# Kernel tuning notes

Measured on AMD Instinct MI355X. Metric: run time of the kernel, lower is better.

Reference implementation:

```python
import math
import jax, jax.numpy as jnp
import numpy as np

D_MODEL = 1024
N_HEADS = 16
D_K = D_MODEL // N_HEADS
THETA = 10000.0
B, S = 2, 2048


def setup_inputs() -> dict:
    key = jax.random.key(0)
    k1, k2, k3 = jax.random.split(key, 3)
    x = jax.random.normal(k1, (B, S, D_MODEL), dtype=jnp.float32)
    token_positions = jnp.arange(B * S, dtype=jnp.int32).reshape(B, S)
    std_qkv = math.sqrt(2.0 / (D_MODEL + 3 * D_MODEL))
    std_o = math.sqrt(2.0 / (D_MODEL + D_MODEL))
    W_qkv = jax.random.truncated_normal(k2, -3.0, 3.0, (3 * D_MODEL, D_MODEL), dtype=jnp.float32) * std_qkv
    W_o = jax.random.truncated_normal(k3, -3.0, 3.0, (D_MODEL, D_MODEL), dtype=jnp.float32) * std_o
    return {"x": x, "W_qkv": W_qkv, "W_o": W_o, "token_positions": token_positions}


def _rope(x, pos):
    # x: (B, H, S, D_K); pos: (B, S) int
    half = D_K // 2
    inv_freq = 1.0 / (THETA ** (jnp.arange(0, D_K, 2, dtype=jnp.float32) / D_K))  # (half,)
    # pos_extended = pos[:, None, :] -> freqs (B, 1, S, half)
    freqs = pos[:, None, :, None].astype(jnp.float32) * inv_freq
    cos, sin = jnp.cos(freqs), jnp.sin(freqs)
    xr = x.reshape(*x.shape[:-1], half, 2)
    x1, x2 = xr[..., 0], xr[..., 1]
    out = jnp.stack([x1 * cos - x2 * sin, x2 * cos + x1 * sin], axis=-1)
    return out.reshape(x.shape)


def reference(x, W_qkv, W_o, token_positions):
    seq_len = x.shape[-2]
    qkv = jnp.einsum('bsi,oi->bso', x, W_qkv)
    q, k, v = jnp.split(qkv, 3, axis=-1)
    # (B, S, H*D) -> (B, H, S, D)
    def to_heads(t):
        return t.reshape(t.shape[0], t.shape[1], N_HEADS, D_K).transpose(0, 2, 1, 3)
    q, k, v = to_heads(q), to_heads(k), to_heads(v)
    q = _rope(q, token_positions)
    k = _rope(k, token_positions)
    scores = jnp.einsum('bhnd,bhmd->bhnm', q, k) / math.sqrt(D_K)
    causal = jnp.tril(jnp.ones((seq_len, seq_len), dtype=bool))
    scores = jnp.where(causal, scores, -jnp.inf)
    attn = jax.nn.softmax(scores, axis=-1)
    out = jnp.einsum('bhnm,bhmd->bhnd', attn, v)
    out = out.transpose(0, 2, 1, 3).reshape(x.shape[0], seq_len, D_MODEL)
    return jnp.einsum('bsi,oi->bso', out, W_o)
```

## Files before the change

kernel.cpp:

```cpp
#include <hip/hip_runtime.h>
#include <cmath>

typedef __bf16 bf16;
typedef bf16 bf16x4 __attribute__((ext_vector_type(4)));
typedef bf16 bf16x8 __attribute__((ext_vector_type(8)));
typedef float f32x4 __attribute__((ext_vector_type(4)));

#define MFMA16(a, b, c) __builtin_amdgcn_mfma_f32_16x16x32_bf16(a, b, c, 0, 0, 0)

#define GLOAD16(g, l)                                                   \
  __builtin_amdgcn_global_load_lds(                                     \
      (const __attribute__((address_space(1))) unsigned int*)(g),       \
      (__attribute__((address_space(3))) unsigned int*)(l), 16, 0, 0)

__global__ __launch_bounds__(256) void cvt_all(
    const float* __restrict__ x, const float* __restrict__ wqkv,
    const float* __restrict__ wo, bf16* __restrict__ xb,
    bf16* __restrict__ wqkvb, bf16* __restrict__ wob) {
  int i = (blockIdx.x * 256 + threadIdx.x) * 4;
  const float* src;
  bf16* dst;
  if (i < (4 << 20)) {
    src = x + i; dst = xb + i;
  } else if (i < (7 << 20)) {
    src = wqkv + (i - (4 << 20)); dst = wqkvb + (i - (4 << 20));
  } else {
    src = wo + (i - (7 << 20)); dst = wob + (i - (7 << 20));
  }
  const f32x4 v = *(const f32x4*)src;
  bf16x4 o = {(bf16)v[0], (bf16)v[1], (bf16)v[2], (bf16)v[3]};
  *(bf16x4*)dst = o;
}

template <int EPI, int BN>
__global__ __launch_bounds__(256) void gemm_nt(
    const bf16* __restrict__ A, const bf16* __restrict__ Bm,
    const int* __restrict__ tokpos,
    bf16* __restrict__ out0, bf16* __restrict__ out1, bf16* __restrict__ out2,
    float* __restrict__ outF, int N) {
  constexpr int NI = BN / 32;
  constexpr int TSTRIDE = 136;
  __shared__ __align__(16) union SMem {
    struct { bf16 A[2][128 * 32]; bf16 B[2][BN * 32]; } st;
    bf16 T[EPI ? 128 * TSTRIDE : 1];
  } sm;
  const int tid = threadIdx.x;
  const int w = tid >> 6, lane = tid & 63, quad = lane >> 4, m16 = lane & 15;
  const int nwg = gridDim.x * gridDim.y;
  int bid = blockIdx.y * gridDim.x + blockIdx.x;
  bid = (bid & 7) * (nwg >> 3) + (bid >> 3);
  const int m0 = (bid / gridDim.x) * 128, n0 = (bid % gridDim.x) * BN;
  const int wm = (w >> 1) * 64, wn = (w & 1) * (BN / 2);

  f32x4 acc[4][NI] = {};

  const int row0 = tid >> 2, ch = tid & 3;
  const bf16* Ag0 = A + (size_t)(m0 + row0) * 1024 + ch * 8;
  const bf16* Ag1 = Ag0 + (size_t)64 * 1024;
  const bf16* Bg0 = Bm + (size_t)(n0 + row0) * 1024 + ch * 8;
  const bf16* Bg1 = Bg0 + (size_t)64 * 1024;

  auto STAGE = [&](int p, int k0) {
    GLOAD16(Ag0 + k0, &sm.st.A[p][tid * 8]);
    GLOAD16(Ag1 + k0, &sm.st.A[p][2048 + tid * 8]);
    GLOAD16(Bg0 + k0, &sm.st.B[p][tid * 8]);
    if constexpr (BN == 128) GLOAD16(Bg1 + k0, &sm.st.B[p][2048 + tid * 8]);
  };

  STAGE(0, 0);
  __syncthreads();

  int p = 0;
  for (int k0 = 0; k0 < 1024; k0 += 32) {
    const bool more = (k0 + 32) < 1024;
    if (more) STAGE(p ^ 1, k0 + 32);
    bf16x8 af[4], bfr[NI];
#pragma unroll
    for (int mi = 0; mi < 4; ++mi)
      af[mi] =
          *(const bf16x8*)(&sm.st.A[p][(wm + mi * 16 + m16) * 32 + quad * 8]);
#pragma unroll
    for (int ni = 0; ni < NI; ++ni)
      bfr[ni] =
          *(const bf16x8*)(&sm.st.B[p][(wn + ni * 16 + m16) * 32 + quad * 8]);
#pragma unroll
    for (int mi = 0; mi < 4; ++mi)
#pragma unroll
      for (int ni = 0; ni < NI; ++ni)
        acc[mi][ni] = MFMA16(af[mi], bfr[ni], acc[mi][ni]);
    if (more) {
      __syncthreads();
      p ^= 1;
    }
  }

  if constexpr (EPI == 0) {
#pragma unroll
    for (int mi = 0; mi < 4; ++mi) {
      int rowb = m0 + wm + mi * 16 + quad * 4;
#pragma unroll
      for (int r = 0; r < 4; ++r) {
        size_t off = (size_t)(rowb + r) * N + n0 + wn;
#pragma unroll
        for (int ni = 0; ni < NI; ++ni)
          outF[off + ni * 16 + m16] = acc[mi][ni][r];
      }
    }
  } else {
    const int secb = n0 >> 10;
    if (secb == 2) {
      __syncthreads();
#pragma unroll
      for (int mi = 0; mi < 4; ++mi) {
        int rlb = wm + mi * 16 + quad * 4;
#pragma unroll
        for (int ni = 0; ni < 4; ++ni) {
          int c = wn + ni * 16 + m16;
          bf16x4 pk = {(bf16)acc[mi][ni][0], (bf16)acc[mi][ni][1],
                       (bf16)acc[mi][ni][2], (bf16)acc[mi][ni][3]};
          *(bf16x4*)(&sm.T[c * TSTRIDE + rlb]) = pk;
        }
      }
      __syncthreads();
      const int bb = m0 >> 11, S0 = m0 & 2047;
      const size_t base = ((size_t)bb * 1024 + (n0 - 2048)) * 2048 + S0;
#pragma unroll
      for (int it = 0; it < 8; ++it) {
        int chunk = it * 256 + tid;
        int c = chunk >> 4, kp = (chunk & 15) * 8;
        bf16x8 v = *(const bf16x8*)(&sm.T[c * TSTRIDE + kp]);
        *(bf16x8*)(out2 + base + (size_t)c * 2048 + kp) = v;
      }
    } else {
      bf16* dst = secb ? out1 : out0;
      const float sc = secb ? 1.0f : 0.125f;
#pragma unroll
      for (int mi = 0; mi < 4; ++mi) {
        int rowb = m0 + wm + mi * 16 + quad * 4;
        int pos4[4];
#pragma unroll
        for (int r = 0; r < 4; ++r) pos4[r] = tokpos[rowb + r];
#pragma unroll
        for (int ni = 0; ni < 4; ++ni) {
          int col = n0 + wn + ni * 16 + m16;
          int f = col & 1023, h = f >> 6, d = f & 63;
          float inv = __expf(-(float)(d & ~1) * (9.2103403719762f / 64.f));
#pragma unroll
          for (int r = 0; r < 4; ++r) {
            float v = acc[mi][ni][r];
            float vp = __shfl_xor(v, 1);
            float ang = (float)pos4[r] * inv;
            float cs, sn;
            __sincosf(ang, &sn, &cs);
            float ov = (d & 1) ? (v * cs + vp * sn) : (v * cs - vp * sn);
            ov *= sc;
            int row = rowb + r;
            int bb = row >> 11, s = row & 2047;
            dst[((size_t)(bb * 16 + h) * 2048 + s) * 64 + d] = (bf16)ov;
          }
        }
      }
    }
  }
}

__global__ __launch_bounds__(256) void attn_kernel(
    const bf16* __restrict__ Q, const bf16* __restrict__ K,
    const bf16* __restrict__ Vt, bf16* __restrict__ O) {
  __shared__ __align__(16) bf16 KP[64 * 64];
  __shared__ __align__(16) bf16 VP[64 * 64];
  __shared__ __align__(16) bf16 PS[4][16 * 64];
  const int tid = threadIdx.x;
  const int w = tid >> 6, lane = tid & 63, quad = lane >> 4, m16 = lane & 15;
  const int h8 = m16 >> 3, ml = m16 & 7;
  const int bh = blockIdx.x;
  const int j = 31 - blockIdx.y;
  const bf16* Qb = Q + (size_t)bh * 2048 * 64;
  const bf16* Kb = K + (size_t)bh * 2048 * 64;
  const bf16* Vb = Vt + (size_t)bh * 64 * 2048;

  const int srow = tid >> 3, sc = (tid & 7) ^ (srow & 7);
  const bf16* Kg = Kb + (size_t)srow * 64 + sc * 8;
  const bf16* Vg = Vb + (size_t)srow * 2048 + sc * 8;
  auto GK = [&](int kt) {
    const bf16* kg = Kg + (size_t)kt * 4096;
    GLOAD16(kg, &KP[tid * 8]);
    GLOAD16(kg + (size_t)32 * 64, &KP[2048 + tid * 8]);
  };
  auto GV = [&](int kt) {
    const bf16* vg = Vg + kt * 64;
    GLOAD16(vg, &VP[tid * 8]);
    GLOAD16(vg + (size_t)32 * 2048, &VP[2048 + tid * 8]);
  };

  const bf16* qrow = Qb + (size_t)(j * 64 + w * 16 + m16) * 64;
  bf16x8 aq[2];
  aq[0] = *(const bf16x8*)(qrow + quad * 8);
  aq[1] = *(const bf16x8*)(qrow + 32 + quad * 8);

  GK(0);
  GV(0);
  __syncthreads();

  f32x4 o[4] = {};
  float l4[4] = {0.f, 0.f, 0.f, 0.f};
  const int qrel = w * 16 + quad * 4;
  bf16* ps = PS[w];

  for (int kt = 0; kt <= j; ++kt) {
    const bool more = kt < j;

    f32x4 sa[4] = {};
    __builtin_amdgcn_s_setprio(1);
#pragma unroll
    for (int kk = 0; kk < 2; ++kk)
#pragma unroll
      for (int ni = 0; ni < 4; ++ni) {
        bf16x8 bk = *(const bf16x8*)(
            &KP[(ni * 16 + m16) * 64 + (((kk * 4 + quad) ^ ml) << 3)]);
        sa[ni] = MFMA16(aq[kk], bk, sa[ni]);
      }
    __builtin_amdgcn_s_setprio(0);

    __syncthreads();
    if (more) GK(kt + 1);

    const bool diag = (kt == j);
#pragma unroll
    for (int r = 0; r < 4; ++r) {
      const int prow = quad * 4 + r;
      const int rb = prow * 64, rx = prow & 7;
#pragma unroll
      for (int ni = 0; ni < 4; ++ni) {
        float pp = exp2f(fmaf(sa[ni][r], 1.44269504f, -11.5415603f));
        if (diag && (ni * 16 + m16) > qrel + r) pp = 0.f;
        l4[r] += pp;
        ps[rb + (((ni * 2 + h8) ^ rx) << 3) + ml] = (bf16)pp;
      }
    }
    bf16x8 ap[2];
#pragma unroll
    for (int kk = 0; kk < 2; ++kk)
      ap[kk] =
          *(const bf16x8*)(&ps[m16 * 64 + (((kk * 4 + quad) ^ ml) << 3)]);
    __builtin_amdgcn_s_setprio(1);
#pragma unroll
    for (int kk = 0; kk < 2; ++kk)
#pragma unroll
      for (int ng = 0; ng < 4; ++ng) {
        bf16x8 bv = *(const bf16x8*)(
            &VP[(ng * 16 + m16) * 64 + (((kk * 4 + quad) ^ ml) << 3)]);
        o[ng] = MFMA16(ap[kk], bv, o[ng]);
      }
    __builtin_amdgcn_s_setprio(0);

    if (more) {
      __syncthreads();
      GV(kt + 1);
    }
  }

  const int b = bh >> 4, hh = bh & 15;
#pragma unroll
  for (int r = 0; r < 4; ++r) {
    float l = l4[r];
    l += __shfl_xor(l, 1);
    l += __shfl_xor(l, 2);
    l += __shfl_xor(l, 4);
    l += __shfl_xor(l, 8);
    float inv_l = 1.f / l;
    int s = j * 64 + w * 16 + quad * 4 + r;
    size_t rowoff = (size_t)(b * 2048 + s) * 1024 + hh * 64;
#pragma unroll
    for (int ng = 0; ng < 4; ++ng)
      O[rowoff + ng * 16 + m16] = (bf16)(o[ng][r] * inv_l);
  }
}

extern "C" void kernel_launch(void* const* d_in, const int* in_sizes, int n_in,
                              void* d_out, int out_size, void* d_ws, size_t ws_size,
                              hipStream_t stream) {
  (void)in_sizes; (void)n_in; (void)out_size; (void)ws_size;
  const float* x = (const float*)d_in[0];
  const float* Wqkv = (const float*)d_in[1];
  const float* Wo = (const float*)d_in[2];
  const int* tokpos = (const int*)d_in[3];
  float* out = (float*)d_out;

  const size_t NEL = (size_t)2 * 16 * 2048 * 64;
  bf16* Qws = (bf16*)d_ws;
  bf16* Kws = Qws + NEL;
  bf16* Vtw = Kws + NEL;
  bf16* Ows = Vtw + NEL;
  bf16* xb  = Ows + NEL;
  bf16* Wqkvb = xb + NEL;
  bf16* Wob = Wqkvb + (size_t)3072 * 1024;

  cvt_all<<<8192, 256, 0, stream>>>(x, Wqkv, Wo, xb, Wqkvb, Wob);

  gemm_nt<1, 128><<<dim3(24, 32), 256, 0, stream>>>(xb, Wqkvb, tokpos, Qws,
                                                    Kws, Vtw, nullptr, 3072);
  attn_kernel<<<dim3(32, 32), 256, 0, stream>>>(Qws, Kws, Vtw, Ows);
  gemm_nt<0, 64><<<dim3(16, 32), 256, 0, stream>>>(Ows, Wob, nullptr, nullptr,
                                                   nullptr, nullptr, out, 1024);
}
```

Baseline: 175.6 us.

## Split long causal attention rows across two blocks with separate reduction kernel

Query tiles in the upper half of the sequence now have their key range split between two blocks. Each block writes unnormalized fp32 partial outputs and row sums into workspace. A new normalize kernel adds the two partials, divides, and writes bf16. This balances work across blocks under the causal mask and adds parallelism, at the cost of extra fp32 global traffic and one more kernel launch.

```diff
diff --git a/kernel.cpp b/kernel.cpp
--- a/kernel.cpp
+++ b/kernel.cpp
@@ -166,7 +166,9 @@
 
 __global__ __launch_bounds__(256) void attn_kernel(
     const bf16* __restrict__ Q, const bf16* __restrict__ K,
-    const bf16* __restrict__ Vt, bf16* __restrict__ O) {
+    const bf16* __restrict__ Vt, bf16* __restrict__ O,
+    float* __restrict__ Oa, float* __restrict__ Ob,
+    float* __restrict__ La, float* __restrict__ Lb) {
   __shared__ __align__(16) bf16 KP[64 * 64];
   __shared__ __align__(16) bf16 VP[64 * 64];
   __shared__ __align__(16) bf16 PS[4][16 * 64];
@@ -174,7 +176,19 @@
   const int w = tid >> 6, lane = tid & 63, quad = lane >> 4, m16 = lane & 15;
   const int h8 = m16 >> 3, ml = m16 & 7;
   const int bh = blockIdx.x;
-  const int j = 31 - blockIdx.y;
+  const int y = blockIdx.y;
+  int j, kt0, kt1;
+  bool split;
+  float *Op, *Lp;
+  if (y < 32) {
+    j = 31 - (y >> 1);
+    const int h = (j + 1) >> 1;
+    split = true;
+    if ((y & 1) == 0) { kt0 = h; kt1 = j; Op = Ob; Lp = Lb; }
+    else              { kt0 = 0; kt1 = h - 1; Op = Oa; Lp = La; }
+  } else {
+    j = 47 - y; kt0 = 0; kt1 = j; split = false; Op = nullptr; Lp = nullptr;
+  }
   const bf16* Qb = Q + (size_t)bh * 2048 * 64;
   const bf16* Kb = K + (size_t)bh * 2048 * 64;
   const bf16* Vb = Vt + (size_t)bh * 64 * 2048;
@@ -198,8 +212,8 @@
   aq[0] = *(const bf16x8*)(qrow + quad * 8);
   aq[1] = *(const bf16x8*)(qrow + 32 + quad * 8);
 
-  GK(0);
-  GV(0);
+  GK(kt0);
+  GV(kt0);
   __syncthreads();
 
   f32x4 o[4] = {};
@@ -207,8 +221,8 @@
   const int qrel = w * 16 + quad * 4;
   bf16* ps = PS[w];
 
-  for (int kt = 0; kt <= j; ++kt) {
-    const bool more = kt < j;
+  for (int kt = kt0; kt <= kt1; ++kt) {
+    const bool more = kt < kt1;
 
     f32x4 sa[4] = {};
     __builtin_amdgcn_s_setprio(1);
@@ -268,13 +282,46 @@
     l += __shfl_xor(l, 2);
     l += __shfl_xor(l, 4);
     l += __shfl_xor(l, 8);
-    float inv_l = 1.f / l;
     int s = j * 64 + w * 16 + quad * 4 + r;
-    size_t rowoff = (size_t)(b * 2048 + s) * 1024 + hh * 64;
-#pragma unroll
-    for (int ng = 0; ng < 4; ++ng)
-      O[rowoff + ng * 16 + m16] = (bf16)(o[ng][r] * inv_l);
-  }
+    if (!split) {
+      float inv_l = 1.f / l;
+      size_t rowoff = (size_t)(b * 2048 + s) * 1024 + hh * 64;
+#pragma unroll
+      for (int ng = 0; ng < 4; ++ng)
+        O[rowoff + ng * 16 + m16] = (bf16)(o[ng][r] * inv_l);
+    } else {
+      int srel = s - 1024;
+      size_t rowoff = (size_t)(b * 1024 + srel) * 1024 + hh * 64;
+#pragma unroll
+      for (int ng = 0; ng < 4; ++ng)
+        Op[rowoff + ng * 16 + m16] = o[ng][r];
+      if (m16 == 0) Lp[(b * 1024 + srel) * 16 + hh] = l;
+    }
+  }
+}
+
+__global__ __launch_bounds__(256) void normalize_k(
+    const float* __restrict__ Oa, const float* __restrict__ Ob,
+    const float* __restrict__ La, const float* __restrict__ Lb,
+    bf16* __restrict__ Ows) {
+  int idx = blockIdx.x * 256 + threadIdx.x;
+  int e = idx * 8;
+  int row = e >> 10;
+  int hh = (e >> 6) & 15;
+  float inv = 1.f / (La[row * 16 + hh] + Lb[row * 16 + hh]);
+  f32x4 a0 = *(const f32x4*)(Oa + e);
+  f32x4 a1 = *(const f32x4*)(Oa + e + 4);
+  f32x4 b0 = *(const f32x4*)(Ob + e);
+  f32x4 b1 = *(const f32x4*)(Ob + e + 4);
+  bf16x8 out;
+#pragma unroll
+  for (int i = 0; i < 4; ++i) {
+    out[i] = (bf16)((a0[i] + b0[i]) * inv);
+    out[4 + i] = (bf16)((a1[i] + b1[i]) * inv);
+  }
+  int b_ = row >> 10, srel = row & 1023;
+  size_t off = ((size_t)(b_ * 2048 + 1024 + srel)) * 1024 + (e & 1023);
+  *(bf16x8*)(Ows + off) = out;
 }
 
 extern "C" void kernel_launch(void* const* d_in, const int* in_sizes, int n_in,
@@ -287,20 +334,27 @@
   const int* tokpos = (const int*)d_in[3];
   float* out = (float*)d_out;
 
-  const size_t NEL = (size_t)2 * 16 * 2048 * 64;
-  bf16* Qws = (bf16*)d_ws;
-  bf16* Kws = Qws + NEL;
-  bf16* Vtw = Kws + NEL;
-  bf16* Ows = Vtw + NEL;
-  bf16* xb  = Ows + NEL;
-  bf16* Wqkvb = xb + NEL;
-  bf16* Wob = Wqkvb + (size_t)3072 * 1024;
+  const size_t Mi = (size_t)1 << 20;
+  bf16* base = (bf16*)d_ws;
+  bf16* xb    = base;
+  bf16* Wqkvb = base + 4 * Mi;
+  bf16* Wob   = base + 8 * Mi;
+  bf16* Qws   = base + 9 * Mi;
+  bf16* Kws   = base + 13 * Mi;
+  bf16* Vtw   = base + 17 * Mi;
+  bf16* Ows   = base + 21 * Mi;
+  float* La   = (float*)(base + 25 * Mi);
+  float* Lb   = La + 32 * 1024;
+  float* Oa   = (float*)base;
+  float* Ob   = Oa + 2 * Mi;
 
   cvt_all<<<8192, 256, 0, stream>>>(x, Wqkv, Wo, xb, Wqkvb, Wob);
 
   gemm_nt<1, 128><<<dim3(24, 32), 256, 0, stream>>>(xb, Wqkvb, tokpos, Qws,
                                                     Kws, Vtw, nullptr, 3072);
-  attn_kernel<<<dim3(32, 32), 256, 0, stream>>>(Qws, Kws, Vtw, Ows);
+  attn_kernel<<<dim3(32, 48), 256, 0, stream>>>(Qws, Kws, Vtw, Ows, Oa, Ob,
+                                                La, Lb);
+  normalize_k<<<1024, 256, 0, stream>>>(Oa, Ob, La, Lb, Ows);
   gemm_nt<0, 64><<<dim3(16, 32), 256, 0, stream>>>(Ows, Wob, nullptr, nullptr,
                                                    nullptr, nullptr, out, 1024);
 }
```

Measured after the change: 190.0 us. +8.2%, slower.
